# Optimization experiments

Measured on AMD Instinct MI355X. Metric: run time of the kernel, lower is better.

## Reference

```python
import jax, jax.numpy as jnp
import numpy as np

N_NODES = 50000
N_EDGES = 800000
IN_C, HID, OUT_C = 128, 128, 16
N_GRAPHS = 128


def setup_inputs() -> dict:
    key = jax.random.key(0)
    ks = jax.random.split(key, 8)
    x = jax.random.normal(ks[0], (N_NODES, IN_C), dtype=jnp.float32)
    edge_index = jax.random.randint(ks[1], (2, N_EDGES), 0, N_NODES, dtype=jnp.int64)
    batch = jnp.sort(jax.random.randint(ks[2], (N_NODES,), 0, N_GRAPHS, dtype=jnp.int64))
    s1 = 1.0 / np.sqrt(IN_C)
    s2 = 1.0 / np.sqrt(HID)
    W1 = jax.random.normal(ks[3], (IN_C, HID), dtype=jnp.float32) * s1
    b1 = jnp.zeros((HID,), dtype=jnp.float32)
    W2 = jax.random.normal(ks[4], (HID, HID), dtype=jnp.float32) * s2
    b2 = jnp.zeros((HID,), dtype=jnp.float32)
    Wfc = jax.random.normal(ks[5], (HID, OUT_C), dtype=jnp.float32) * s2
    bfc = jnp.zeros((OUT_C,), dtype=jnp.float32)
    return {"x": x, "edge_index": edge_index, "batch": batch,
            "W1": W1, "b1": b1, "W2": W2, "b2": b2, "Wfc": Wfc, "bfc": bfc}


def _gcn_conv(x, W, b, src, dst, deg_inv_sqrt, n_nodes):
    # linear transform first (PyG order), then normalized sparse aggregation
    h = x @ W  # [N, H]
    norm = deg_inv_sqrt[src] * deg_inv_sqrt[dst]  # [E+N] (self-loops appended)
    msgs = h[src] * norm[:, None]  # [E+N, H] dominant gather
    agg = jax.ops.segment_sum(msgs, dst, num_segments=n_nodes)
    return agg + b


def reference(x, edge_index, batch, W1, b1, W2, b2, Wfc, bfc):
    n = x.shape[0]
    loops = jnp.arange(n, dtype=edge_index.dtype)
    src = jnp.concatenate([edge_index[0], loops])
    dst = jnp.concatenate([edge_index[1], loops])
    # symmetric normalization with self-loops: deg computed on dst
    deg = jax.ops.segment_sum(jnp.ones_like(src, dtype=x.dtype), dst, num_segments=n)
    deg_inv_sqrt = jnp.where(deg > 0, jax.lax.rsqrt(jnp.maximum(deg, 1.0)), 0.0)

    h = jax.nn.relu(_gcn_conv(x, W1, b1, src, dst, deg_inv_sqrt, n))
    h = jax.nn.relu(_gcn_conv(h, W2, b2, src, dst, deg_inv_sqrt, n))

    # global mean pool over graph ids
    sums = jax.ops.segment_sum(h, batch, num_segments=N_GRAPHS)
    counts = jax.ops.segment_sum(jnp.ones((n,), dtype=h.dtype), batch, num_segments=N_GRAPHS)
    pooled = sums / jnp.maximum(counts, 1.0)[:, None]  # [G, H]

    logits = pooled @ Wfc + bfc  # [G, OUT_C]
    return jax.nn.log_softmax(logits, axis=1)
```

## Files before the change

kernel.cpp:

```cpp
#include <hip/hip_runtime.h>

#define N_NODES  50000
#define N_EDGES  800000
#define HID      128
#define OUT_C    16
#define N_GRAPHS 128
#define MAXDEG   64
#define NSLICE   6250
#define EPB      8192
#define FILLB    784
#define PREPB    128
#define GEMMB    782
#define PAD      136

typedef __attribute__((ext_vector_type(8))) short bf16x8;
typedef __attribute__((ext_vector_type(4))) float f32x4;
typedef __attribute__((ext_vector_type(8))) unsigned short us8;
typedef __attribute__((ext_vector_type(4))) unsigned short us4;

__device__ __forceinline__ unsigned short f2bf(float f) {
  unsigned u = __float_as_uint(f);
  u += 0x7fffu + ((u >> 16) & 1u);
  return (unsigned short)(u >> 16);
}

__global__ __launch_bounds__(256) void mega0_kernel(
    const int* __restrict__ src, const int* __restrict__ dst,
    int* __restrict__ deg, unsigned short* __restrict__ ell,
    const int* __restrict__ batch, int* __restrict__ start,
    const float* __restrict__ W1, const float* __restrict__ W2,
    unsigned short* __restrict__ wt1, unsigned short* __restrict__ wt2) {
  int b = blockIdx.x;
  if (b < FILLB) {
    const int slice = b & 7;
    const int e0 = (b >> 3) * EPB;
    const int e1 = min(e0 + EPB, N_EDGES);
    const unsigned lo = slice * NSLICE;
    for (int e = e0 + threadIdx.x; e < e1; e += 256) {
      int d = __builtin_nontemporal_load(dst + e);
      if ((unsigned)(d - lo) < (unsigned)NSLICE) {
        int p = atomicAdd(&deg[d], 1);
        if (p < MAXDEG) ell[(d << 6) + p] = (unsigned short)src[e];
      }
    }
  } else if (b == FILLB) {
    int t = threadIdx.x;
    if (t <= N_GRAPHS) {
      int lo = 0, hi = N_NODES;
      while (lo < hi) {
        int mid = (lo + hi) >> 1;
        if (batch[mid] < t) lo = mid + 1; else hi = mid;
      }
      start[t] = lo;
    }
  } else {
    int idx = (b - FILLB - 1) * 256 + threadIdx.x;
    int sel = idx >> 14;
    int r = idx & 16383;
    int k = r >> 7, n = r & 127;
    const float* W = sel ? W2 : W1;
    unsigned short* wt = sel ? wt2 : wt1;
    wt[n * HID + k] = f2bf(W[k * HID + n]);
  }
}

__device__ __forceinline__ void gemm_compute_store(
    unsigned short* sA, unsigned short* sW, unsigned short* __restrict__ T,
    int base) {
  const int tid = threadIdx.x;
  const int lane = tid & 63;
  const int w = tid >> 6;
  const int l15 = lane & 15;
  const int quad = lane >> 4;
  __syncthreads();

  f32x4 acc[4][2];
#pragma unroll
  for (int nt = 0; nt < 4; ++nt)
#pragma unroll
    for (int c = 0; c < 2; ++c) acc[nt][c] = (f32x4)(0.f);

  const int ct0 = w * 2;
#pragma unroll
  for (int ks = 0; ks < 4; ++ks) {
    int koff = ks * 32 + quad * 8;
    bf16x8 a[4], bfr[2];
#pragma unroll
    for (int nt = 0; nt < 4; ++nt)
      a[nt] = *(const bf16x8*)(sA + (nt * 16 + l15) * PAD + koff);
#pragma unroll
    for (int c = 0; c < 2; ++c)
      bfr[c] = *(const bf16x8*)(sW + ((ct0 + c) * 16 + l15) * PAD + koff);
#pragma unroll
    for (int nt = 0; nt < 4; ++nt)
#pragma unroll
      for (int c = 0; c < 2; ++c)
        acc[nt][c] = __builtin_amdgcn_mfma_f32_16x16x32_bf16(a[nt], bfr[c], acc[nt][c], 0, 0, 0);
  }
  __syncthreads();

#pragma unroll
  for (int nt = 0; nt < 4; ++nt)
#pragma unroll
    for (int c = 0; c < 2; ++c)
#pragma unroll
      for (int r = 0; r < 4; ++r)
        sA[(nt * 16 + quad * 4 + r) * PAD + (ct0 + c) * 16 + l15] = f2bf(acc[nt][c][r]);
  __syncthreads();
#pragma unroll
  for (int i = 0; i < 4; ++i) {
    int idx = tid + i * 256;
    int nrow = idx >> 4;
    int col = (idx & 15) * 8;
    int node = base + nrow;
    if (node < N_NODES)
      *(us8*)(T + (size_t)node * HID + col) = *(const us8*)(sA + nrow * PAD + col);
  }
}

__device__ __forceinline__ void stage_w(unsigned short* sW,
                                        const unsigned short* __restrict__ Wt) {
#pragma unroll
  for (int i = 0; i < 8; ++i) {
    int idx = threadIdx.x + i * 256;
    int row = idx >> 4;
    int col = (idx & 15) * 8;
    *(us8*)(sW + row * PAD + col) = *(const us8*)(Wt + row * HID + col);
  }
}

__global__ __launch_bounds__(256) void gemm_f32_kernel(
    const float* __restrict__ H, const unsigned short* __restrict__ Wt,
    unsigned short* __restrict__ T) {
  __shared__ unsigned short smem[192 * PAD];
  unsigned short* sA = smem;
  unsigned short* sW = smem + 64 * PAD;
  stage_w(sW, Wt);
  const int base = blockIdx.x * 64;
#pragma unroll
  for (int i = 0; i < 8; ++i) {
    int idx = threadIdx.x + i * 256;
    int nrow = idx >> 5;
    int c4 = (idx & 31) * 4;
    float4 v = make_float4(0.f, 0.f, 0.f, 0.f);
    int node = base + nrow;
    if (node < N_NODES) v = *(const float4*)(H + (size_t)node * HID + c4);
    us4 b;
    b.x = f2bf(v.x); b.y = f2bf(v.y); b.z = f2bf(v.z); b.w = f2bf(v.w);
    *(us4*)(sA + nrow * PAD + c4) = b;
  }
  gemm_compute_store(sA, sW, T, base);
}

__global__ __launch_bounds__(256) void gemm_bf16_kernel(
    const unsigned short* __restrict__ Hb, const unsigned short* __restrict__ Wt,
    unsigned short* __restrict__ T) {
  __shared__ unsigned short smem[192 * PAD];
  unsigned short* sA = smem;
  unsigned short* sW = smem + 64 * PAD;
  stage_w(sW, Wt);
  const int base = blockIdx.x * 64;
#pragma unroll
  for (int i = 0; i < 4; ++i) {
    int idx = threadIdx.x + i * 256;
    int nrow = idx >> 4;
    int col = (idx & 15) * 8;
    us8 v = (us8)(0);
    int node = base + nrow;
    if (node < N_NODES) v = *(const us8*)(Hb + (size_t)node * HID + col);
    *(us8*)(sA + nrow * PAD + col) = v;
  }
  gemm_compute_store(sA, sW, T, base);
}

__global__ __launch_bounds__(256) void aggregate_kernel(
    const unsigned int* __restrict__ Tb, const unsigned short* __restrict__ ell,
    const int* __restrict__ deg, const float* __restrict__ bias,
    unsigned int* __restrict__ Hb) {
  int node = (blockIdx.x * blockDim.x + threadIdx.x) >> 6;
  int lane = threadIdx.x & 63;
  if (node >= N_NODES) return;
  int dn = deg[node];
  float dd = rsqrtf((float)dn + 1.0f);
  float2 b = ((const float2*)bias)[lane];
  unsigned sv = Tb[(size_t)node * 64 + lane];
  float wself = dd * dd;
  float ax = __int_as_float(sv << 16) * wself;
  float ay = __int_as_float(sv & 0xffff0000u) * wself;
  int m = min(dn, MAXDEG);
  int s0 = node << 6;
  int sidx = 0; float wv = 0.f;
  if (lane < m) {
    sidx = (int)ell[s0 + lane];
    wv = rsqrtf((float)deg[sidx] + 1.0f) * dd;
  }
  int j = 0;
  for (; j + 8 <= m; j += 8) {
#pragma unroll
    for (int q = 0; q < 8; ++q) {
      int s = __builtin_amdgcn_readlane(sidx, j + q);
      float w = __int_as_float(__builtin_amdgcn_readlane(__float_as_int(wv), j + q));
      unsigned t = Tb[(size_t)s * 64 + lane];
      ax += w * __int_as_float(t << 16);
      ay += w * __int_as_float(t & 0xffff0000u);
    }
  }
  for (; j < m; ++j) {
    int s = __builtin_amdgcn_readlane(sidx, j);
    float w = __int_as_float(__builtin_amdgcn_readlane(__float_as_int(wv), j));
    unsigned t = Tb[(size_t)s * 64 + lane];
    ax += w * __int_as_float(t << 16);
    ay += w * __int_as_float(t & 0xffff0000u);
  }
  float ox = fmaxf(ax + b.x, 0.f);
  float oy = fmaxf(ay + b.y, 0.f);
  Hb[(size_t)node * 64 + lane] =
      (unsigned)f2bf(ox) | ((unsigned)f2bf(oy) << 16);
}

__global__ __launch_bounds__(256) void pool_head_kernel(
    const unsigned int* __restrict__ Hb, const int* __restrict__ start,
    const float* __restrict__ Wfc, const float* __restrict__ bfc,
    float* __restrict__ out) {
  __shared__ float2 red[4][64];
  __shared__ float spool[HID];
  int g = blockIdx.x;
  int n0 = start[g], n1 = start[g + 1];
  int lane = threadIdx.x & 63, w = threadIdx.x >> 6;
  float ax = 0.f, ay = 0.f;
  for (int n = n0 + w; n < n1; n += 4) {
    unsigned h = Hb[(size_t)n * 64 + lane];
    ax += __int_as_float(h << 16);
    ay += __int_as_float(h & 0xffff0000u);
  }
  red[w][lane] = make_float2(ax, ay);
  __syncthreads();
  if (threadIdx.x < 64) {
    float2 a = red[0][lane], b1 = red[1][lane], c = red[2][lane], d = red[3][lane];
    float inv = 1.0f / fmaxf((float)(n1 - n0), 1.0f);
    spool[lane * 2]     = (a.x + b1.x + c.x + d.x) * inv;
    spool[lane * 2 + 1] = (a.y + b1.y + c.y + d.y) * inv;
  }
  __syncthreads();
  if (threadIdx.x < 64) {
    int o = lane & 15;
    float part = 0.f;
    for (int k = (lane >> 4); k < HID; k += 4)
      part += spool[k] * Wfc[k * OUT_C + o];
    part += __shfl_xor(part, 16);
    part += __shfl_xor(part, 32);
    float logit = part + bfc[o];
    float m = logit;
#pragma unroll
    for (int d = 8; d >= 1; d >>= 1) m = fmaxf(m, __shfl_xor(m, d, 16));
    float e = __expf(logit - m);
    float s = e;
#pragma unroll
    for (int d = 8; d >= 1; d >>= 1) s += __shfl_xor(s, d, 16);
    float r = logit - m - __logf(s);
    if (lane < 16) out[g * OUT_C + o] = r;
  }
}

extern "C" void kernel_launch(void* const* d_in, const int* in_sizes, int n_in,
                              void* d_out, int out_size, void* d_ws, size_t ws_size,
                              hipStream_t stream) {
  const float* x    = (const float*)d_in[0];
  const int*   ei   = (const int*)d_in[1];
  const int*   batch= (const int*)d_in[2];
  const float* W1   = (const float*)d_in[3];
  const float* b1   = (const float*)d_in[4];
  const float* W2   = (const float*)d_in[5];
  const float* b2   = (const float*)d_in[6];
  const float* Wfc  = (const float*)d_in[7];
  const float* bfc  = (const float*)d_in[8];
  float* out = (float*)d_out;
  const int* src = ei;
  const int* dst = ei + N_EDGES;

  char* p = (char*)d_ws;
  auto alloc = [&](size_t bytes) { char* r = p; p += (bytes + 255) & ~255ull; return r; };
  int*   degI   = (int*)alloc((size_t)N_NODES * 4);
  int*   start  = (int*)alloc((N_GRAPHS + 1) * 4);
  unsigned short* ell = (unsigned short*)alloc((size_t)N_NODES * MAXDEG * 2);
  unsigned short* wt1 = (unsigned short*)alloc((size_t)HID * HID * 2);
  unsigned short* wt2 = (unsigned short*)alloc((size_t)HID * HID * 2);
  unsigned short* T   = (unsigned short*)alloc((size_t)N_NODES * HID * 2);
  unsigned short* Hb  = (unsigned short*)alloc((size_t)N_NODES * HID * 2);

  hipMemsetAsync(degI, 0, (size_t)N_NODES * 4, stream);

  int agg_blocks = (N_NODES * 64 + 255) / 256;

  mega0_kernel<<<FILLB + 1 + PREPB, 256, 0, stream>>>(src, dst, degI, ell,
                                                      batch, start, W1, W2, wt1, wt2);
  gemm_f32_kernel<<<GEMMB, 256, 0, stream>>>(x, wt1, T);
  aggregate_kernel<<<agg_blocks, 256, 0, stream>>>((const unsigned int*)T, ell, degI, b1,
                                                   (unsigned int*)Hb);
  gemm_bf16_kernel<<<GEMMB, 256, 0, stream>>>(Hb, wt2, T);
  aggregate_kernel<<<agg_blocks, 256, 0, stream>>>((const unsigned int*)T, ell, degI, b2,
                                                   (unsigned int*)Hb);
  pool_head_kernel<<<N_GRAPHS, 256, 0, stream>>>((const unsigned int*)Hb, start,
                                                 Wfc, bfc, out);
}
```

Baseline: 266.8 us.

## Fuse first GEMM into edge-fill kernel and read fp32 weights directly

Removes the separate weight-transpose/convert pass and the staged bf16 weight tiles in shared memory. Each wave now loads its B fragments straight from the fp32 weight matrix in global memory with strided scalar loads and converts them to bf16 in registers. The first layer's x@W1 GEMM blocks are merged into the same launch as the ELL fill and graph-start search, so the GEMM runs concurrently with the atomic-heavy fill and one launch is saved. The cost is redundant, uncoalesced weight loads in every block, relying on L2 to serve them, and a larger mixed kernel whose shared memory is also reserved by the fill blocks.

```diff
diff --git a/kernel.cpp b/kernel.cpp
--- a/kernel.cpp
+++ b/kernel.cpp
@@ -9,7 +9,6 @@
 #define NSLICE   6250
 #define EPB      8192
 #define FILLB    784
-#define PREPB    128
 #define GEMMB    782
 #define PAD      136
 
@@ -24,12 +23,87 @@
   return (unsigned short)(u >> 16);
 }
 
-__global__ __launch_bounds__(256) void mega0_kernel(
+__device__ __forceinline__ void gemm_compute_store(
+    unsigned short* sA, const float* __restrict__ W,
+    unsigned short* __restrict__ T, int base) {
+  const int tid = threadIdx.x;
+  const int lane = tid & 63;
+  const int w = tid >> 6;
+  const int l15 = lane & 15;
+  const int quad = lane >> 4;
+  __syncthreads();
+
+  f32x4 acc[4][2];
+#pragma unroll
+  for (int nt = 0; nt < 4; ++nt)
+#pragma unroll
+    for (int c = 0; c < 2; ++c) acc[nt][c] = (f32x4)(0.f);
+
+  const int ct0 = w * 2;
+  const int ncol = ct0 * 16 + l15;
+#pragma unroll
+  for (int ks = 0; ks < 4; ++ks) {
+    const int koff = ks * 32 + quad * 8;
+    bf16x8 a[4], bfr[2];
+#pragma unroll
+    for (int c = 0; c < 2; ++c) {
+      const float* wp = W + (size_t)koff * HID + ncol + c * 16;
+#pragma unroll
+      for (int j = 0; j < 8; ++j) bfr[c][j] = (short)f2bf(wp[(size_t)j * HID]);
+    }
+#pragma unroll
+    for (int nt = 0; nt < 4; ++nt)
+      a[nt] = *(const bf16x8*)(sA + (nt * 16 + l15) * PAD + koff);
+#pragma unroll
+    for (int nt = 0; nt < 4; ++nt)
+#pragma unroll
+      for (int c = 0; c < 2; ++c)
+        acc[nt][c] = __builtin_amdgcn_mfma_f32_16x16x32_bf16(a[nt], bfr[c], acc[nt][c], 0, 0, 0);
+  }
+  __syncthreads();
+
+#pragma unroll
+  for (int nt = 0; nt < 4; ++nt)
+#pragma unroll
+    for (int c = 0; c < 2; ++c)
+#pragma unroll
+      for (int r = 0; r < 4; ++r)
+        sA[(nt * 16 + quad * 4 + r) * PAD + (ct0 + c) * 16 + l15] = f2bf(acc[nt][c][r]);
+  __syncthreads();
+#pragma unroll
+  for (int i = 0; i < 4; ++i) {
+    int idx = tid + i * 256;
+    int nrow = idx >> 4;
+    int col = (idx & 15) * 8;
+    int node = base + nrow;
+    if (node < N_NODES)
+      *(us8*)(T + (size_t)node * HID + col) = *(const us8*)(sA + nrow * PAD + col);
+  }
+}
+
+__device__ __forceinline__ void stage_a_f32(unsigned short* sA,
+                                            const float* __restrict__ H, int base) {
+#pragma unroll
+  for (int i = 0; i < 8; ++i) {
+    int idx = threadIdx.x + i * 256;
+    int nrow = idx >> 5;
+    int c4 = (idx & 31) * 4;
+    float4 v = make_float4(0.f, 0.f, 0.f, 0.f);
+    int node = base + nrow;
+    if (node < N_NODES) v = *(const float4*)(H + (size_t)node * HID + c4);
+    us4 b;
+    b.x = f2bf(v.x); b.y = f2bf(v.y); b.z = f2bf(v.z); b.w = f2bf(v.w);
+    *(us4*)(sA + nrow * PAD + c4) = b;
+  }
+}
+
+__global__ __launch_bounds__(256) void mega_kernel(
     const int* __restrict__ src, const int* __restrict__ dst,
     int* __restrict__ deg, unsigned short* __restrict__ ell,
     const int* __restrict__ batch, int* __restrict__ start,
-    const float* __restrict__ W1, const float* __restrict__ W2,
-    unsigned short* __restrict__ wt1, unsigned short* __restrict__ wt2) {
+    const float* __restrict__ x, const float* __restrict__ W1,
+    unsigned short* __restrict__ T) {
+  __shared__ unsigned short sA[64 * PAD];
   int b = blockIdx.x;
   if (b < FILLB) {
     const int slice = b & 7;
@@ -54,111 +128,16 @@
       start[t] = lo;
     }
   } else {
-    int idx = (b - FILLB - 1) * 256 + threadIdx.x;
-    int sel = idx >> 14;
-    int r = idx & 16383;
-    int k = r >> 7, n = r & 127;
-    const float* W = sel ? W2 : W1;
-    unsigned short* wt = sel ? wt2 : wt1;
-    wt[n * HID + k] = f2bf(W[k * HID + n]);
-  }
-}
-
-__device__ __forceinline__ void gemm_compute_store(
-    unsigned short* sA, unsigned short* sW, unsigned short* __restrict__ T,
-    int base) {
-  const int tid = threadIdx.x;
-  const int lane = tid & 63;
-  const int w = tid >> 6;
-  const int l15 = lane & 15;
-  const int quad = lane >> 4;
-  __syncthreads();
-
-  f32x4 acc[4][2];
-#pragma unroll
-  for (int nt = 0; nt < 4; ++nt)
-#pragma unroll
-    for (int c = 0; c < 2; ++c) acc[nt][c] = (f32x4)(0.f);
-
-  const int ct0 = w * 2;
-#pragma unroll
-  for (int ks = 0; ks < 4; ++ks) {
-    int koff = ks * 32 + quad * 8;
-    bf16x8 a[4], bfr[2];
-#pragma unroll
-    for (int nt = 0; nt < 4; ++nt)
-      a[nt] = *(const bf16x8*)(sA + (nt * 16 + l15) * PAD + koff);
-#pragma unroll
-    for (int c = 0; c < 2; ++c)
-      bfr[c] = *(const bf16x8*)(sW + ((ct0 + c) * 16 + l15) * PAD + koff);
-#pragma unroll
-    for (int nt = 0; nt < 4; ++nt)
-#pragma unroll
-      for (int c = 0; c < 2; ++c)
-        acc[nt][c] = __builtin_amdgcn_mfma_f32_16x16x32_bf16(a[nt], bfr[c], acc[nt][c], 0, 0, 0);
-  }
-  __syncthreads();
-
-#pragma unroll
-  for (int nt = 0; nt < 4; ++nt)
-#pragma unroll
-    for (int c = 0; c < 2; ++c)
-#pragma unroll
-      for (int r = 0; r < 4; ++r)
-        sA[(nt * 16 + quad * 4 + r) * PAD + (ct0 + c) * 16 + l15] = f2bf(acc[nt][c][r]);
-  __syncthreads();
-#pragma unroll
-  for (int i = 0; i < 4; ++i) {
-    int idx = tid + i * 256;
-    int nrow = idx >> 4;
-    int col = (idx & 15) * 8;
-    int node = base + nrow;
-    if (node < N_NODES)
-      *(us8*)(T + (size_t)node * HID + col) = *(const us8*)(sA + nrow * PAD + col);
-  }
-}
-
-__device__ __forceinline__ void stage_w(unsigned short* sW,
-                                        const unsigned short* __restrict__ Wt) {
-#pragma unroll
-  for (int i = 0; i < 8; ++i) {
-    int idx = threadIdx.x + i * 256;
-    int row = idx >> 4;
-    int col = (idx & 15) * 8;
-    *(us8*)(sW + row * PAD + col) = *(const us8*)(Wt + row * HID + col);
-  }
-}
-
-__global__ __launch_bounds__(256) void gemm_f32_kernel(
-    const float* __restrict__ H, const unsigned short* __restrict__ Wt,
+    const int base = (b - FILLB - 1) * 64;
+    stage_a_f32(sA, x, base);
+    gemm_compute_store(sA, W1, T, base);
+  }
+}
+
+__global__ __launch_bounds__(256) void gemm_bf16_kernel(
+    const unsigned short* __restrict__ Hb, const float* __restrict__ W,
     unsigned short* __restrict__ T) {
-  __shared__ unsigned short smem[192 * PAD];
-  unsigned short* sA = smem;
-  unsigned short* sW = smem + 64 * PAD;
-  stage_w(sW, Wt);
-  const int base = blockIdx.x * 64;
-#pragma unroll
-  for (int i = 0; i < 8; ++i) {
-    int idx = threadIdx.x + i * 256;
-    int nrow = idx >> 5;
-    int c4 = (idx & 31) * 4;
-    float4 v = make_float4(0.f, 0.f, 0.f, 0.f);
-    int node = base + nrow;
-    if (node < N_NODES) v = *(const float4*)(H + (size_t)node * HID + c4);
-    us4 b;
-    b.x = f2bf(v.x); b.y = f2bf(v.y); b.z = f2bf(v.z); b.w = f2bf(v.w);
-    *(us4*)(sA + nrow * PAD + c4) = b;
-  }
-  gemm_compute_store(sA, sW, T, base);
-}
-
-__global__ __launch_bounds__(256) void gemm_bf16_kernel(
-    const unsigned short* __restrict__ Hb, const unsigned short* __restrict__ Wt,
-    unsigned short* __restrict__ T) {
-  __shared__ unsigned short smem[192 * PAD];
-  unsigned short* sA = smem;
-  unsigned short* sW = smem + 64 * PAD;
-  stage_w(sW, Wt);
+  __shared__ unsigned short sA[64 * PAD];
   const int base = blockIdx.x * 64;
 #pragma unroll
   for (int i = 0; i < 4; ++i) {
@@ -170,7 +149,7 @@
     if (node < N_NODES) v = *(const us8*)(Hb + (size_t)node * HID + col);
     *(us8*)(sA + nrow * PAD + col) = v;
   }
-  gemm_compute_store(sA, sW, T, base);
+  gemm_compute_store(sA, W, T, base);
 }
 
 __global__ __launch_bounds__(256) void aggregate_kernel(
@@ -283,8 +262,6 @@
   int*   degI   = (int*)alloc((size_t)N_NODES * 4);
   int*   start  = (int*)alloc((N_GRAPHS + 1) * 4);
   unsigned short* ell = (unsigned short*)alloc((size_t)N_NODES * MAXDEG * 2);
-  unsigned short* wt1 = (unsigned short*)alloc((size_t)HID * HID * 2);
-  unsigned short* wt2 = (unsigned short*)alloc((size_t)HID * HID * 2);
   unsigned short* T   = (unsigned short*)alloc((size_t)N_NODES * HID * 2);
   unsigned short* Hb  = (unsigned short*)alloc((size_t)N_NODES * HID * 2);
 
@@ -292,12 +269,11 @@
 
   int agg_blocks = (N_NODES * 64 + 255) / 256;
 
-  mega0_kernel<<<FILLB + 1 + PREPB, 256, 0, stream>>>(src, dst, degI, ell,
-                                                      batch, start, W1, W2, wt1, wt2);
-  gemm_f32_kernel<<<GEMMB, 256, 0, stream>>>(x, wt1, T);
+  mega_kernel<<<FILLB + 1 + GEMMB, 256, 0, stream>>>(src, dst, degI, ell,
+                                                     batch, start, x, W1, T);
   aggregate_kernel<<<agg_blocks, 256, 0, stream>>>((const unsigned int*)T, ell, degI, b1,
                                                    (unsigned int*)Hb);
-  gemm_bf16_kernel<<<GEMMB, 256, 0, stream>>>(Hb, wt2, T);
+  gemm_bf16_kernel<<<GEMMB, 256, 0, stream>>>(Hb, W2, T);
   aggregate_kernel<<<agg_blocks, 256, 0, stream>>>((const unsigned int*)T, ell, degI, b2,
                                                    (unsigned int*)Hb);
   pool_head_kernel<<<N_GRAPHS, 256, 0, stream>>>((const unsigned int*)Hb, start,
```

Result: faster. 255.5 us (-4.2%).
